# Kernel tuning notes

Measured on AMD Instinct MI355X. Metric: run time of the kernel, lower is better.

The kernel has to match this reference:

```python
import jax, jax.numpy as jnp
import numpy as np

D_MODEL, HEAD_DIM = 1024, 128

def setup_inputs() -> dict:
    key = jax.random.key(0)
    kx, kq, kk, kv = jax.random.split(key, 4)
    x = jax.random.normal(kx, (4, 4096, D_MODEL), dtype=jnp.float32)
    s = 1.0 / np.sqrt(D_MODEL)
    Wq = jax.random.normal(kq, (D_MODEL, HEAD_DIM), dtype=jnp.float32) * s
    Wk = jax.random.normal(kk, (D_MODEL, HEAD_DIM), dtype=jnp.float32) * s
    Wv = jax.random.normal(kv, (D_MODEL, HEAD_DIM), dtype=jnp.float32) * s
    return {"x": x, "Wq": Wq, "Wk": Wk, "Wv": Wv}

def reference(x, Wq, Wk, Wv):
    # x: [b, s, d_model]; Wq/Wk/Wv: [d_model, head_dim]
    q = jnp.einsum('bsd,dh->bsh', x, Wq)
    k = jnp.einsum('bsd,dh->bsh', x, Wk)
    v = jnp.einsum('bsd,dh->bsh', x, Wv)
    seq = x.shape[1]
    scale = 1.0 / jnp.sqrt(jnp.asarray(q.shape[-1], q.dtype))
    scores = jnp.einsum('bqh,bkh->bqk', q, k) * scale  # [b, s, s]
    causal = jnp.tril(jnp.ones((seq, seq), dtype=bool))
    scores = jnp.where(causal, scores, jnp.asarray(-jnp.inf, scores.dtype))
    attn = jax.nn.softmax(scores, axis=-1)
    return jnp.einsum('bqk,bkh->bqh', attn, v)
```

## Files before the change

kernel.cpp:

```cpp
#include <hip/hip_runtime.h>
#include <hip/hip_bf16.h>
#include <math.h>

#define D_MODEL 1024
#define HD 128
#define SEQ 4096

typedef __bf16 bf16x8 __attribute__((ext_vector_type(8)));
typedef float f32x4 __attribute__((ext_vector_type(4)));
typedef unsigned int u32;
typedef u32 u32x4 __attribute__((ext_vector_type(4)));

__device__ __forceinline__ unsigned short f2bf(float f) {
    union { float f; u32 u; } c; c.f = f;
    u32 u = c.u;
    u = (u + 0x7fffu + ((u >> 16) & 1u)) >> 16;
    return (unsigned short)u;
}
__device__ __forceinline__ u32 pk2(float a, float b) {
    __hip_bfloat162 h = __float22bfloat162_rn(make_float2(a, b));
    union { __hip_bfloat162 h; u32 u; } c; c.h = h; return c.u;
}
__device__ __forceinline__ void dma16(void* lds, const void* g) {
    __builtin_amdgcn_global_load_lds(
        (const __attribute__((address_space(1))) u32*)g,
        (__attribute__((address_space(3))) u32*)lds, 16, 0, 0);
}
__device__ __forceinline__ void drain_dma() {
    __builtin_amdgcn_s_waitcnt(0x0F70);
}

__global__ __launch_bounds__(256)
void wt_kernel(const float* __restrict__ Wq, const float* __restrict__ Wk,
               const float* __restrict__ Wv, unsigned short* __restrict__ Wt) {
    __shared__ float wsf[64][129];
    const int t = threadIdx.x;
    const int k0 = blockIdx.x * 64;
    const int mat = blockIdx.y;
    const float* W = (mat == 0) ? Wq : (mat == 1) ? Wk : Wv;
    const float sc = (mat == 0) ? (0.08838834764831845f * 1.4426950408889634f) : 1.0f;
    {
        const int r = t >> 2, c = (t & 3) * 32;
        const float* src = W + (size_t)(k0 + r) * HD + c;
        #pragma unroll
        for (int j = 0; j < 32; j += 4)
            *reinterpret_cast<f32x4*>(&wsf[r][c + j]) = *reinterpret_cast<const f32x4*>(src + j);
    }
    __syncthreads();
    const int n = t >> 1, ks = (t & 1) * 32;
    u32 ow[16];
    #pragma unroll
    for (int j = 0; j < 16; ++j)
        ow[j] = pk2(wsf[ks + 2 * j][n] * sc, wsf[ks + 2 * j + 1][n] * sc);
    unsigned short* dst = Wt + (size_t)(mat * HD + n) * D_MODEL + k0 + ks;
    #pragma unroll
    for (int j = 0; j < 4; ++j)
        *reinterpret_cast<u32x4*>(dst + j * 8) = (u32x4){ow[4*j], ow[4*j+1], ow[4*j+2], ow[4*j+3]};
}

__global__ __launch_bounds__(256)
void proj_kernel(const float* __restrict__ x, const unsigned short* __restrict__ Wt,
                 unsigned short* __restrict__ Qb, unsigned short* __restrict__ Kb,
                 unsigned short* __restrict__ Vt) {
    __shared__ __align__(1024) char ps[32768];
    const int t = threadIdx.x;
    const int w = t >> 6, l = t & 63, li = l & 15, g2 = l >> 4;
    const int id = blockIdx.x;
    const int grp = id / 24, win = id % 24;
    const int nbase = (win >> 3) * 128;
    const int rowbase = (grp * 8 + (win & 7)) * 64;

    f32x4 acc[8];
    #pragma unroll
    for (int nt = 0; nt < 8; ++nt) acc[nt] = (f32x4){0.f, 0.f, 0.f, 0.f};

    const int lrow = l >> 3;
    const int xg = (l & 7) ^ (lrow & 6);
    const int wgr = (l & 7) ^ lrow;
    const int wrow_add = (wgr >> 2) << 6;
    const int wkc = (wgr & 3) * 8;

    auto stage = [&](int k0, int buf) {
        #pragma unroll
        for (int j = 0; j < 2; ++j) {
            int r0 = w * 16 + 8 * j;
            dma16(ps + buf * 8192 + r0 * 128,
                  x + (size_t)(rowbase + r0 + lrow) * D_MODEL + k0 + xg * 4);
            dma16(ps + 16384 + buf * 8192 + r0 * 128,
                  Wt + (size_t)(nbase + r0 + lrow + wrow_add) * D_MODEL + k0 + wkc);
        }
    };

    stage(0, 0);
    for (int it = 0; it < 32; ++it) {
        const int buf = it & 1;
        drain_dma();
        __syncthreads();
        if (it + 1 < 32) stage((it + 1) * 32, buf ^ 1);
        const char* xb = ps + buf * 8192 + (w * 16 + li) * 128 + (((2 * g2) ^ (li & 6)) * 16);
        f32x4 x0 = *reinterpret_cast<const f32x4*>(xb);
        f32x4 x1 = *reinterpret_cast<const f32x4*>(xb + 16);
        union { u32 d[4]; bf16x8 v; } cva;
        cva.d[0] = pk2(x0[0], x0[1]); cva.d[1] = pk2(x0[2], x0[3]);
        cva.d[2] = pk2(x1[0], x1[1]); cva.d[3] = pk2(x1[2], x1[3]);
        bf16x8 af = cva.v;
        #pragma unroll
        for (int nt = 0; nt < 8; ++nt) {
            bf16x8 bfr = *reinterpret_cast<const bf16x8*>(
                ps + 16384 + buf * 8192 + ((nt & 3) * 16 + li) * 128 +
                ((((nt >> 2) * 4 + g2) ^ (li & 7)) * 16));
            acc[nt] = __builtin_amdgcn_mfma_f32_16x16x32_bf16(af, bfr, acc[nt], 0, 0, 0);
        }
    }

    if (nbase < 256) {
        unsigned short* P = nbase ? Kb : Qb;
        #pragma unroll
        for (int nt = 0; nt < 8; ++nt)
            #pragma unroll
            for (int r = 0; r < 4; ++r) {
                int grow = rowbase + w * 16 + g2 * 4 + r;
                P[(size_t)grow * HD + nt * 16 + li] = f2bf(acc[nt][r]);
            }
    } else {
        int grow0 = rowbase + w * 16 + g2 * 4;
        int b_ = grow0 >> 12, s_ = grow0 & 4095;
        #pragma unroll
        for (int nt = 0; nt < 8; ++nt) {
            ushort4 s4;
            s4.x = f2bf(acc[nt][0]); s4.y = f2bf(acc[nt][1]);
            s4.z = f2bf(acc[nt][2]); s4.w = f2bf(acc[nt][3]);
            *reinterpret_cast<ushort4*>(&Vt[((size_t)b_ * HD + nt * 16 + li) * SEQ + s_]) = s4;
        }
    }
}

__global__ __launch_bounds__(256, 2)
void attn_kernel(const unsigned short* __restrict__ Qb, const unsigned short* __restrict__ Kb,
                 const unsigned short* __restrict__ Vt, float* __restrict__ outO,
                 unsigned short* __restrict__ Obf, float* __restrict__ Lbuf) {
    __shared__ __align__(1024) char smem[73728];
    const int t = threadIdx.x;
    const int w = t >> 6, l = t & 63, li = l & 15, g2 = l >> 4;
    const int qh = w >> 1, kh = w & 1;
    const int b = blockIdx.x & 3;
    const int u = blockIdx.x >> 2;
    const int g = 63 - (u >> 2);
    const int c = u & 3;
    const int R = g + 1;
    const int ts = (c * R) >> 2, te = ((c + 1) * R) >> 2;
    const int q0 = g * 64;
    const size_t rowb = (size_t)b * SEQ;
    const int koff = kh * 32;

    const unsigned short* KbB = Kb + rowb * HD;
    const unsigned short* VtB = Vt + (size_t)b * HD * SEQ;
    const int vgran = ((l & 7) ^ (l >> 3)) * 8;

    auto stage = [&](int it, char* base) {
        const int j0 = it * 64;
        #pragma unroll
        for (int j = 0; j < 4; ++j) {
            int rK = w * 16 + 4 * j + (l >> 4);
            dma16(base + (w * 16 + 4 * j) * 256,
                  KbB + (size_t)(j0 + rK) * 128 + (((l & 15) ^ (rK & 7)) * 8));
            int rV = w * 32 + 8 * j + (l >> 3);
            dma16(base + 16384 + (w * 32 + 8 * j) * 128,
                  VtB + (size_t)rV * SEQ + j0 + vgran);
        }
    };

    bf16x8 qf[2][4];
    #pragma unroll
    for (int qt = 0; qt < 2; ++qt)
        #pragma unroll
        for (int ks = 0; ks < 4; ++ks)
            qf[qt][ks] = *reinterpret_cast<const bf16x8*>(
                Qb + (rowb + q0 + qh * 32 + qt * 16 + li) * HD + ks * 32 + g2 * 8);

    f32x4 acco[2][8];
    #pragma unroll
    for (int qt = 0; qt < 2; ++qt)
        #pragma unroll
        for (int dt = 0; dt < 8; ++dt) acco[qt][dt] = (f32x4){0.f, 0.f, 0.f, 0.f};
    float ls[2][4] = {{0.f,0.f,0.f,0.f},{0.f,0.f,0.f,0.f}};

    const int gV = ((4 * kh + g2) ^ (li & 7)) * 16;

    if (ts < te) stage(ts, smem);
    for (int it = ts; it < te; ++it) {
        char* cbuf = smem + ((it - ts) & 1) * 32768;
        char* nbuf = smem + (((it - ts) & 1) ^ 1) * 32768;
        drain_dma();
        __syncthreads();
        if (it + 1 < te) stage(it + 1, nbuf);

        f32x4 accs[2][2];
        #pragma unroll
        for (int qt = 0; qt < 2; ++qt)
            #pragma unroll
            for (int kt = 0; kt < 2; ++kt) accs[qt][kt] = (f32x4){0.f, 0.f, 0.f, 0.f};
        #pragma unroll
        for (int kt = 0; kt < 2; ++kt) {
            const char* kb = cbuf + (koff + kt * 16 + li) * 256;
            #pragma unroll
            for (int ks = 0; ks < 4; ++ks) {
                bf16x8 kf = *reinterpret_cast<const bf16x8*>(kb + (((4 * ks + g2) ^ (li & 7)) * 16));
                accs[0][kt] = __builtin_amdgcn_mfma_f32_16x16x32_bf16(qf[0][ks], kf, accs[0][kt], 0, 0, 0);
                accs[1][kt] = __builtin_amdgcn_mfma_f32_16x16x32_bf16(qf[1][ks], kf, accs[1][kt], 0, 0, 0);
            }
        }

        const bool masked = (it == g);
        #pragma unroll
        for (int qt = 0; qt < 2; ++qt)
            #pragma unroll
            for (int kt = 0; kt < 2; ++kt)
                #pragma unroll
                for (int r = 0; r < 4; ++r) {
                    float s = accs[qt][kt][r];
                    if (masked && (koff + kt * 16 + li > qh * 32 + qt * 16 + g2 * 4 + r))
                        s = -INFINITY;
                    float p = __builtin_amdgcn_exp2f(s - 16.0f);
                    ls[qt][r] += p;
                    int prow = qh * 32 + qt * 16 + g2 * 4 + r;
                    int gw = (4 * kh + 2 * kt + (li >> 3)) ^ ((4 * g2 + r) & 7);
                    *reinterpret_cast<unsigned short*>(
                        smem + 65536 + prow * 128 + gw * 16 + (li & 7) * 2) = f2bf(p);
                }

        bf16x8 pf0 = *reinterpret_cast<const bf16x8*>(smem + 65536 + (qh * 32 + li) * 128 + gV);
        bf16x8 pf1 = *reinterpret_cast<const bf16x8*>(smem + 65536 + (qh * 32 + 16 + li) * 128 + gV);
        #pragma unroll
        for (int dt = 0; dt < 8; ++dt) {
            bf16x8 vf = *reinterpret_cast<const bf16x8*>(cbuf + 16384 + (dt * 16 + li) * 128 + gV);
            acco[0][dt] = __builtin_amdgcn_mfma_f32_16x16x32_bf16(pf0, vf, acco[0][dt], 0, 0, 0);
            acco[1][dt] = __builtin_amdgcn_mfma_f32_16x16x32_bf16(pf1, vf, acco[1][dt], 0, 0, 0);
        }
    }

    #pragma unroll
    for (int d = 1; d < 16; d <<= 1)
        #pragma unroll
        for (int qt = 0; qt < 2; ++qt)
            #pragma unroll
            for (int r = 0; r < 4; ++r)
                ls[qt][r] += __shfl_xor(ls[qt][r], d);

    float (*Osum)[132] = (float(*)[132])smem;
    float* Lsh = (float*)(smem + 33792);
    __syncthreads();
    if (kh == 0) {
        #pragma unroll
        for (int qt = 0; qt < 2; ++qt) {
            #pragma unroll
            for (int dt = 0; dt < 8; ++dt)
                #pragma unroll
                for (int r = 0; r < 4; ++r)
                    Osum[qh * 32 + qt * 16 + g2 * 4 + r][dt * 16 + li] = acco[qt][dt][r];
            if (li == 0)
                #pragma unroll
                for (int r = 0; r < 4; ++r)
                    Lsh[qh * 32 + qt * 16 + g2 * 4 + r] = ls[qt][r];
        }
    }
    __syncthreads();
    if (kh == 1) {
        #pragma unroll
        for (int qt = 0; qt < 2; ++qt) {
            #pragma unroll
            for (int dt = 0; dt < 8; ++dt)
                #pragma unroll
                for (int r = 0; r < 4; ++r)
                    Osum[qh * 32 + qt * 16 + g2 * 4 + r][dt * 16 + li] += acco[qt][dt][r];
            if (li == 0)
                #pragma unroll
                for (int r = 0; r < 4; ++r)
                    Lsh[64 + qh * 32 + qt * 16 + g2 * 4 + r] = ls[qt][r];
        }
    }
    __syncthreads();

    if (t < 64)
        Lbuf[(size_t)c * 16384 + rowb + q0 + t] = Lsh[t] + Lsh[64 + t];
    #pragma unroll
    for (int k = 0; k < 8; ++k) {
        int idx = t + k * 256;
        int row = idx >> 5, col = (idx & 31) * 4;
        f32x4 o = *reinterpret_cast<const f32x4*>(&Osum[row][col]);
        size_t grow = rowb + q0 + row;
        if (c == 3) {
            *reinterpret_cast<f32x4*>(&outO[grow * HD + col]) = o;
        } else {
            union { u32 d[2]; uint2 v; } pkd;
            pkd.d[0] = pk2(o[0], o[1]); pkd.d[1] = pk2(o[2], o[3]);
            *reinterpret_cast<uint2*>(&Obf[(size_t)c * 2097152 + grow * HD + col]) = pkd.v;
        }
    }
}

__global__ __launch_bounds__(256)
void merge_kernel(float* __restrict__ outO, const unsigned short* __restrict__ Obf,
                  const float* __restrict__ Lbuf) {
    int tid = blockIdx.x * 256 + threadIdx.x;
    #pragma unroll
    for (int k = 0; k < 4; ++k) {
        int idx = tid + k * 131072;
        int row = idx >> 5, col = (idx & 31) * 4;
        float lsum = Lbuf[row] + Lbuf[16384 + row] + Lbuf[32768 + row] + Lbuf[49152 + row];
        float inv = 1.f / lsum;
        f32x4 o = *reinterpret_cast<const f32x4*>(&outO[(size_t)row * HD + col]);
        #pragma unroll
        for (int cc = 0; cc < 3; ++cc) {
            ushort4 uu = *reinterpret_cast<const ushort4*>(
                &Obf[(size_t)cc * 2097152 + (size_t)row * HD + col]);
            union { u32 u; float f; } a, b2, c2, d2;
            a.u = (u32)uu.x << 16; b2.u = (u32)uu.y << 16;
            c2.u = (u32)uu.z << 16; d2.u = (u32)uu.w << 16;
            o[0] += a.f; o[1] += b2.f; o[2] += c2.f; o[3] += d2.f;
        }
        #pragma unroll
        for (int j = 0; j < 4; ++j) o[j] *= inv;
        *reinterpret_cast<f32x4*>(&outO[(size_t)row * HD + col]) = o;
    }
}

extern "C" void kernel_launch(void* const* d_in, const int* in_sizes, int n_in,
                              void* d_out, int out_size, void* d_ws, size_t ws_size,
                              hipStream_t stream) {
    const float* x  = (const float*)d_in[0];
    const float* Wq = (const float*)d_in[1];
    const float* Wk = (const float*)d_in[2];
    const float* Wv = (const float*)d_in[3];
    float* out = (float*)d_out;

    char* ws = (char*)d_ws;
    unsigned short* Qb  = (unsigned short*)(ws);
    unsigned short* Kb  = (unsigned short*)(ws + ((size_t)4  << 20));
    unsigned short* Vt  = (unsigned short*)(ws + ((size_t)8  << 20));
    unsigned short* Wt  = (unsigned short*)(ws + ((size_t)12 << 20));
    unsigned short* Obf = (unsigned short*)(ws + ((size_t)13 << 20));
    float*          Lb  = (float*)(ws + ((size_t)25 << 20));

    wt_kernel   <<<dim3(16, 3), dim3(256), 0, stream>>>(Wq, Wk, Wv, Wt);
    proj_kernel <<<dim3(768),   dim3(256), 0, stream>>>(x, Wt, Qb, Kb, Vt);
    attn_kernel <<<dim3(1024),  dim3(256), 0, stream>>>(Qb, Kb, Vt, out, Obf, Lb);
    merge_kernel<<<dim3(512),   dim3(256), 0, stream>>>(out, Obf, Lb);
}
```

Baseline: 169.5 us.

## Triple-buffer projection loads and transpose MFMA operands in attention for vectorized P/O stores

```diff
diff --git a/kernel.cpp b/kernel.cpp
--- a/kernel.cpp
+++ b/kernel.cpp
@@ -26,9 +26,8 @@
         (const __attribute__((address_space(1))) u32*)g,
         (__attribute__((address_space(3))) u32*)lds, 16, 0, 0);
 }
-__device__ __forceinline__ void drain_dma() {
-    __builtin_amdgcn_s_waitcnt(0x0F70);
-}
+__device__ __forceinline__ void drain_dma()  { __builtin_amdgcn_s_waitcnt(0x0F70); }
+__device__ __forceinline__ void drain_dma4() { __builtin_amdgcn_s_waitcnt(0x0F74); }
 
 __global__ __launch_bounds__(256)
 void wt_kernel(const float* __restrict__ Wq, const float* __restrict__ Wk,
@@ -62,7 +61,7 @@
 void proj_kernel(const float* __restrict__ x, const unsigned short* __restrict__ Wt,
                  unsigned short* __restrict__ Qb, unsigned short* __restrict__ Kb,
                  unsigned short* __restrict__ Vt) {
-    __shared__ __align__(1024) char ps[32768];
+    __shared__ __align__(1024) char ps[49152];
     const int t = threadIdx.x;
     const int w = t >> 6, l = t & 63, li = l & 15, g2 = l >> 4;
     const int id = blockIdx.x;
@@ -86,17 +85,18 @@
             int r0 = w * 16 + 8 * j;
             dma16(ps + buf * 8192 + r0 * 128,
                   x + (size_t)(rowbase + r0 + lrow) * D_MODEL + k0 + xg * 4);
-            dma16(ps + 16384 + buf * 8192 + r0 * 128,
+            dma16(ps + 24576 + buf * 8192 + r0 * 128,
                   Wt + (size_t)(nbase + r0 + lrow + wrow_add) * D_MODEL + k0 + wkc);
         }
     };
 
     stage(0, 0);
+    stage(32, 1);
     for (int it = 0; it < 32; ++it) {
-        const int buf = it & 1;
-        drain_dma();
+        const int buf = it % 3;
+        if (it < 31) drain_dma4(); else drain_dma();
         __syncthreads();
-        if (it + 1 < 32) stage((it + 1) * 32, buf ^ 1);
+        if (it + 2 < 32) stage((it + 2) * 32, (it + 2) % 3);
         const char* xb = ps + buf * 8192 + (w * 16 + li) * 128 + (((2 * g2) ^ (li & 6)) * 16);
         f32x4 x0 = *reinterpret_cast<const f32x4*>(xb);
         f32x4 x1 = *reinterpret_cast<const f32x4*>(xb + 16);
@@ -107,7 +107,7 @@
         #pragma unroll
         for (int nt = 0; nt < 8; ++nt) {
             bf16x8 bfr = *reinterpret_cast<const bf16x8*>(
-                ps + 16384 + buf * 8192 + ((nt & 3) * 16 + li) * 128 +
+                ps + 24576 + buf * 8192 + ((nt & 3) * 16 + li) * 128 +
                 ((((nt >> 2) * 4 + g2) ^ (li & 7)) * 16));
             acc[nt] = __builtin_amdgcn_mfma_f32_16x16x32_bf16(af, bfr, acc[nt], 0, 0, 0);
         }
@@ -183,7 +183,7 @@
     for (int qt = 0; qt < 2; ++qt)
         #pragma unroll
         for (int dt = 0; dt < 8; ++dt) acco[qt][dt] = (f32x4){0.f, 0.f, 0.f, 0.f};
-    float ls[2][4] = {{0.f,0.f,0.f,0.f},{0.f,0.f,0.f,0.f}};
+    float ls[2] = {0.f, 0.f};
 
     const int gV = ((4 * kh + g2) ^ (li & 7)) * 16;
 
@@ -206,78 +206,82 @@
             #pragma unroll
             for (int ks = 0; ks < 4; ++ks) {
                 bf16x8 kf = *reinterpret_cast<const bf16x8*>(kb + (((4 * ks + g2) ^ (li & 7)) * 16));
-                accs[0][kt] = __builtin_amdgcn_mfma_f32_16x16x32_bf16(qf[0][ks], kf, accs[0][kt], 0, 0, 0);
-                accs[1][kt] = __builtin_amdgcn_mfma_f32_16x16x32_bf16(qf[1][ks], kf, accs[1][kt], 0, 0, 0);
+                accs[0][kt] = __builtin_amdgcn_mfma_f32_16x16x32_bf16(kf, qf[0][ks], accs[0][kt], 0, 0, 0);
+                accs[1][kt] = __builtin_amdgcn_mfma_f32_16x16x32_bf16(kf, qf[1][ks], accs[1][kt], 0, 0, 0);
             }
         }
 
         const bool masked = (it == g);
         #pragma unroll
-        for (int qt = 0; qt < 2; ++qt)
-            #pragma unroll
-            for (int kt = 0; kt < 2; ++kt)
+        for (int qt = 0; qt < 2; ++qt) {
+            const int prow = qh * 32 + qt * 16 + li;
+            #pragma unroll
+            for (int kt = 0; kt < 2; ++kt) {
+                float p[4];
                 #pragma unroll
                 for (int r = 0; r < 4; ++r) {
                     float s = accs[qt][kt][r];
-                    if (masked && (koff + kt * 16 + li > qh * 32 + qt * 16 + g2 * 4 + r))
-                        s = -INFINITY;
-                    float p = __builtin_amdgcn_exp2f(s - 16.0f);
-                    ls[qt][r] += p;
-                    int prow = qh * 32 + qt * 16 + g2 * 4 + r;
-                    int gw = (4 * kh + 2 * kt + (li >> 3)) ^ ((4 * g2 + r) & 7);
-                    *reinterpret_cast<unsigned short*>(
-                        smem + 65536 + prow * 128 + gw * 16 + (li & 7) * 2) = f2bf(p);
+                    if (masked && (koff + kt * 16 + g2 * 4 + r > prow)) s = -INFINITY;
+                    p[r] = __builtin_amdgcn_exp2f(s - 16.0f);
+                    ls[qt] += p[r];
                 }
-
-        bf16x8 pf0 = *reinterpret_cast<const bf16x8*>(smem + 65536 + (qh * 32 + li) * 128 + gV);
-        bf16x8 pf1 = *reinterpret_cast<const bf16x8*>(smem + 65536 + (qh * 32 + 16 + li) * 128 + gV);
+                union { u32 d[2]; uint2 v; } pw;
+                pw.d[0] = pk2(p[0], p[1]); pw.d[1] = pk2(p[2], p[3]);
+                int gr = (kh * 4 + kt * 2 + (g2 >> 1)) ^ (prow & 7);
+                *reinterpret_cast<uint2*>(
+                    smem + 65536 + prow * 128 + gr * 16 + (g2 & 1) * 8) = pw.v;
+            }
+        }
+
+        bf16x8 pb[2];
+        #pragma unroll
+        for (int qt = 0; qt < 2; ++qt) {
+            const int prow = qh * 32 + qt * 16 + li;
+            pb[qt] = *reinterpret_cast<const bf16x8*>(
+                smem + 65536 + prow * 128 + (((kh * 4 + g2) ^ (prow & 7)) * 16));
+        }
         #pragma unroll
         for (int dt = 0; dt < 8; ++dt) {
-            bf16x8 vf = *reinterpret_cast<const bf16x8*>(cbuf + 16384 + (dt * 16 + li) * 128 + gV);
-            acco[0][dt] = __builtin_amdgcn_mfma_f32_16x16x32_bf16(pf0, vf, acco[0][dt], 0, 0, 0);
-            acco[1][dt] = __builtin_amdgcn_mfma_f32_16x16x32_bf16(pf1, vf, acco[1][dt], 0, 0, 0);
-        }
-    }
-
-    #pragma unroll
-    for (int d = 1; d < 16; d <<= 1)
-        #pragma unroll
-        for (int qt = 0; qt < 2; ++qt)
-            #pragma unroll
-            for (int r = 0; r < 4; ++r)
-                ls[qt][r] += __shfl_xor(ls[qt][r], d);
+            bf16x8 va = *reinterpret_cast<const bf16x8*>(cbuf + 16384 + (dt * 16 + li) * 128 + gV);
+            acco[0][dt] = __builtin_amdgcn_mfma_f32_16x16x32_bf16(va, pb[0], acco[0][dt], 0, 0, 0);
+            acco[1][dt] = __builtin_amdgcn_mfma_f32_16x16x32_bf16(va, pb[1], acco[1][dt], 0, 0, 0);
+        }
+    }
+
+    #pragma unroll
+    for (int qt = 0; qt < 2; ++qt) {
+        ls[qt] += __shfl_xor(ls[qt], 16);
+        ls[qt] += __shfl_xor(ls[qt], 32);
+    }
 
     float (*Osum)[132] = (float(*)[132])smem;
     float* Lsh = (float*)(smem + 33792);
     __syncthreads();
+    if (l < 16) {
+        Lsh[kh * 64 + qh * 32 + l]      = ls[0];
+        Lsh[kh * 64 + qh * 32 + 16 + l] = ls[1];
+    }
     if (kh == 0) {
         #pragma unroll
-        for (int qt = 0; qt < 2; ++qt) {
+        for (int qt = 0; qt < 2; ++qt)
             #pragma unroll
             for (int dt = 0; dt < 8; ++dt)
-                #pragma unroll
-                for (int r = 0; r < 4; ++r)
-                    Osum[qh * 32 + qt * 16 + g2 * 4 + r][dt * 16 + li] = acco[qt][dt][r];
-            if (li == 0)
-                #pragma unroll
-                for (int r = 0; r < 4; ++r)
-                    Lsh[qh * 32 + qt * 16 + g2 * 4 + r] = ls[qt][r];
-        }
+                *reinterpret_cast<f32x4*>(
+                    &Osum[qh * 32 + qt * 16 + li][dt * 16 + g2 * 4]) = acco[qt][dt];
     }
     __syncthreads();
     if (kh == 1) {
         #pragma unroll
-        for (int qt = 0; qt < 2; ++qt) {
-            #pragma unroll
-            for (int dt = 0; dt < 8; ++dt)
+        for (int qt = 0; qt < 2; ++qt)
+            #pragma unroll
+            for (int dt = 0; dt < 8; ++dt) {
+                f32x4* p = reinterpret_cast<f32x4*>(
+                    &Osum[qh * 32 + qt * 16 + li][dt * 16 + g2 * 4]);
+                f32x4 v = *p;
                 #pragma unroll
-                for (int r = 0; r < 4; ++r)
-                    Osum[qh * 32 + qt * 16 + g2 * 4 + r][dt * 16 + li] += acco[qt][dt][r];
-            if (li == 0)
-                #pragma unroll
-                for (int r = 0; r < 4; ++r)
-                    Lsh[64 + qh * 32 + qt * 16 + g2 * 4 + r] = ls[qt][r];
-        }
+                for (int j = 0; j < 4; ++j) v[j] += acco[qt][dt][j];
+                *p = v;
+            }
     }
     __syncthreads();
 
```

Result: faster. 165.9 us (-2.1%).
